# Kernel optimization log

Hardware: AMD Instinct MI355X
Metric: run time of the kernel (lower is better)

## Reference

```python
import jax, jax.numpy as jnp
import numpy as np

CHANNELS = 64
NUM_HEADS = 8
HEAD_DIM = 64
TOTAL_DIM = NUM_HEADS * HEAD_DIM  # 512
FF_DIM = 1024


def setup_inputs() -> dict:
    key = jax.random.key(0)
    ks = jax.random.split(key, 11)
    def lin(kw, kb, out_d, in_d):
        s = 1.0 / np.sqrt(in_d)
        W = jax.random.uniform(kw, (out_d, in_d), jnp.float32, -s, s)
        b = jax.random.uniform(kb, (out_d,), jnp.float32, -s, s)
        return W, b
    x = jax.random.normal(ks[0], (2, CHANNELS, 64, 32), jnp.float32)
    Wq, bq = lin(ks[1], ks[2], TOTAL_DIM, CHANNELS)
    Wk, bk = lin(ks[3], ks[4], TOTAL_DIM, CHANNELS)
    Wv, bv = lin(ks[5], ks[6], TOTAL_DIM, CHANNELS)
    W1, b1 = lin(ks[7], ks[8], FF_DIM, TOTAL_DIM)
    W2, b2 = lin(ks[9], ks[10], CHANNELS, FF_DIM)
    return {"x": x, "Wq": Wq, "bq": bq, "Wk": Wk, "bk": bk,
            "Wv": Wv, "bv": bv, "W1": W1, "b1": b1, "W2": W2, "b2": b2}


def reference(x, Wq, bq, Wk, bk, Wv, bv, W1, b1, W2, b2):
    N, C, H, W = x.shape
    S = H * W
    # [N, S, C]
    x_flat = x.reshape(N, C, S).transpose(0, 2, 1)
    def heads(y):  # [N,S,total] -> [N,h,S,d]
        return y.reshape(N, S, NUM_HEADS, HEAD_DIM).transpose(0, 2, 1, 3)
    Q = heads(x_flat @ Wq.T + bq)
    K = heads(x_flat @ Wk.T + bk)
    V = heads(x_flat @ Wv.T + bv)
    scale = HEAD_DIM ** 0.5
    logits = jnp.einsum('bhqd,bhkd->bhqk', Q, K) / scale
    attn = jax.nn.softmax(logits, axis=-1)
    out = jnp.einsum('bhqk,bhkd->bhqd', attn, V)
    out = out.transpose(0, 2, 1, 3).reshape(N, S, TOTAL_DIM)
    ff = jax.nn.relu(out @ W1.T + b1) @ W2.T + b2
    y = x_flat + ff
    return y.transpose(0, 2, 1).reshape(N, C, H, W)
```

## Files before the change

### kernel.cpp

```cpp
#include <hip/hip_runtime.h>
#include <hip/hip_bf16.h>

constexpr int S  = 2048;
constexpr int C  = 64;
constexpr int NH = 8;
constexpr int HD = 64;
constexpr int TD = 512;
constexpr int FF = 1024;
constexpr int NB = 2;
constexpr int SPLIT  = 4;
constexpr int KTILES = S / SPLIT / 64;

typedef __bf16 bf16x8 __attribute__((ext_vector_type(8)));
typedef float  f32x4  __attribute__((ext_vector_type(4)));

__device__ __forceinline__ f32x4 mfma16(bf16x8 a, bf16x8 b, f32x4 c) {
  return __builtin_amdgcn_mfma_f32_16x16x32_bf16(a, b, c, 0, 0, 0);
}

__device__ __forceinline__ unsigned int pack_bf2(float a, float b) {
  unsigned short ua = __builtin_bit_cast(unsigned short, (__bf16)a);
  unsigned short ub = __builtin_bit_cast(unsigned short, (__bf16)b);
  return (unsigned int)ua | ((unsigned int)ub << 16);
}

__device__ __forceinline__ float bfu2f(unsigned short u) {
  return __builtin_bit_cast(float, (unsigned int)u << 16);
}


__device__ __forceinline__ void cvt_panel(const float* __restrict__ src,
                                          __hip_bfloat16* __restrict__ dst,
                                          int off, int Wd) {
  const int w8 = Wd >> 3;
  const int r  = off / w8;
  const int k8 = off - r * w8;
  const float4 v0 = *(const float4*)(src + (size_t)r * Wd + k8 * 8);
  const float4 v1 = *(const float4*)(src + (size_t)r * Wd + k8 * 8 + 4);
  const int dc = ((r >> 4) * (Wd >> 5) + (k8 >> 2)) * 64 + (k8 & 3) * 16 + (r & 15);
  uint4 pk;
  pk.x = pack_bf2(v0.x, v0.y); pk.y = pack_bf2(v0.z, v0.w);
  pk.z = pack_bf2(v1.x, v1.y); pk.w = pack_bf2(v1.z, v1.w);
  *(uint4*)&dst[dc * 8] = pk;
}

__global__ __launch_bounds__(256) void k_pre(
    const float* __restrict__ Wq, const float* __restrict__ Wk,
    const float* __restrict__ Wv, const float* __restrict__ W1,
    const float* __restrict__ W2, const float* __restrict__ x,
    __hip_bfloat16* __restrict__ Wqf, __hip_bfloat16* __restrict__ Wkf,
    __hip_bfloat16* __restrict__ Wvf, __hip_bfloat16* __restrict__ W1f,
    __hip_bfloat16* __restrict__ W2f, __hip_bfloat16* __restrict__ xbf) {
  const int b = blockIdx.x;
  if (b < 336) {
    const int q = b * 256 + threadIdx.x;
    if      (q < 4096)  cvt_panel(Wq, Wqf, q,         C);
    else if (q < 8192)  cvt_panel(Wk, Wkf, q - 4096,  C);
    else if (q < 12288) cvt_panel(Wv, Wvf, q - 8192,  C);
    else if (q < 77824) cvt_panel(W1, W1f, q - 12288, TD);
    else                cvt_panel(W2, W2f, q - 77824, FF);
  } else {
    const int id = (b - 336) * 256 + threadIdx.x;
    const int k8 = id >> 12;
    const int m  = id & 4095;
    const int n  = m >> 11, s = m & 2047;
    float v[8];
    #pragma unroll
    for (int j = 0; j < 8; ++j)
      v[j] = x[(size_t)(n * C + k8 * 8 + j) * S + s];
    const int p = m >> 4, ks = k8 >> 2, l = (m & 15) + (k8 & 3) * 16;
    uint4 pk;
    pk.x = pack_bf2(v[0], v[1]); pk.y = pack_bf2(v[2], v[3]);
    pk.z = pack_bf2(v[4], v[5]); pk.w = pack_bf2(v[6], v[7]);
    *(uint4*)&xbf[((p * 2 + ks) * 64 + l) * 8] = pk;
  }
}

__global__ __launch_bounds__(256) void k_qkv(
    const __hip_bfloat16* __restrict__ xbf,
    const __hip_bfloat16* __restrict__ Wqf, const float* __restrict__ bq,
    const __hip_bfloat16* __restrict__ Wkf, const float* __restrict__ bk,
    const __hip_bfloat16* __restrict__ Wvf, const float* __restrict__ bv,
    __hip_bfloat16* __restrict__ Qf, __hip_bfloat16* __restrict__ Kf,
    __hip_bfloat16* __restrict__ Vf) {
  const int t = threadIdx.x, w = t >> 6, l = t & 63;
  const int c = l & 15, g = l >> 4;
  const int m0 = blockIdx.y * 64 + w * 16;
  const int xcol = blockIdx.x, which = xcol >> 3, h = xcol & 7;

  const __hip_bfloat16* Wf = (which == 0) ? Wqf : (which == 1) ? Wkf : Wvf;
  const float*        bias = (which == 0) ? bq  : (which == 1) ? bk  : bv;

  f32x4 acc[4];
  #pragma unroll
  for (int i = 0; i < 4; ++i) acc[i] = f32x4{0.f, 0.f, 0.f, 0.f};

  #pragma unroll
  for (int ks = 0; ks < 2; ++ks) {
    const bf16x8 af = *(const bf16x8*)&xbf[(((m0 >> 4) * 2 + ks) * 64 + l) * 8];
    #pragma unroll
    for (int dt = 0; dt < 4; ++dt) {
      const bf16x8 wf =
          *(const bf16x8*)&Wf[(((h * 4 + dt) * 2 + ks) * 64 + l) * 8];
      acc[dt] = mfma16(wf, af, acc[dt]);
    }
  }

  const int m = m0 + c;
  const int nb_ = m >> 11, s = m & 2047;
  const size_t hbq = (size_t)(nb_ * 8 + h) * (S * HD);

  if (which < 2) {
    const float scl = (which == 0) ? 0.1803368801f : 1.0f;
    __hip_bfloat16* Of = ((which == 0) ? Qf : Kf) + hbq;
    const int sp16 = s >> 4;
    #pragma unroll
    for (int dt = 0; dt < 4; ++dt) {
      const int ks = dt >> 1;
      const int lw = c + ((dt & 1) * 2 + (g >> 1)) * 16;
      const int jb = (4 * g) & 7;
      const int d0 = dt * 16 + 4 * g;
      uint2 pk;
      pk.x = pack_bf2((acc[dt][0] + bias[h * 64 + d0 + 0]) * scl,
                      (acc[dt][1] + bias[h * 64 + d0 + 1]) * scl);
      pk.y = pack_bf2((acc[dt][2] + bias[h * 64 + d0 + 2]) * scl,
                      (acc[dt][3] + bias[h * 64 + d0 + 3]) * scl);
      *(uint2*)&Of[((sp16 * 2 + ks) * 64 + lw) * 8 + jb] = pk;
    }
  } else {
    __hip_bfloat16* Vfh = Vf + hbq;
    const int kc = s >> 5, jj = s & 7, lhi = ((s & 31) >> 3) * 16;
    #pragma unroll
    for (int dt = 0; dt < 4; ++dt)
      #pragma unroll
      for (int r = 0; r < 4; ++r) {
        const float v = acc[dt][r] + bias[h * 64 + dt * 16 + 4 * g + r];
        Vfh[((dt * 64 + kc) * 64 + (4 * g + r + lhi)) * 8 + jj] =
            __float2bfloat16(v);
      }
  }
}

__global__ __launch_bounds__(128, 4) void k_attn(
    const __hip_bfloat16* __restrict__ Qf,
    const __hip_bfloat16* __restrict__ Kf,
    const __hip_bfloat16* __restrict__ Vf,
    __hip_bfloat16* __restrict__ Opart, float* __restrict__ Lpart) {
  __shared__ unsigned short P_lds[2][2][2][16][72];

  const int t = threadIdx.x, w = t >> 6, l = t & 63;
  const int c = l & 15, g = l >> 4;
  const int bid = blockIdx.x;
  const int hb  = bid & 15;
  const int sp  = (bid >> 4) & (SPLIT - 1);
  const int q0  = (bid >> 6) * 64 + w * 32;
  const size_t hbase = (size_t)hb * (S * HD);

  bf16x8 qf[2][2];
  const int qp0 = q0 >> 4;
  #pragma unroll
  for (int qq = 0; qq < 2; ++qq)
    #pragma unroll
    for (int ks = 0; ks < 2; ++ks)
      qf[qq][ks] =
          *(const bf16x8*)&Qf[hbase + (((qp0 + qq) * 2 + ks) * 64 + l) * 8];

  f32x4 o[2][4];
  #pragma unroll
  for (int qq = 0; qq < 2; ++qq)
    #pragma unroll
    for (int i = 0; i < 4; ++i) o[qq][i] = f32x4{0.f, 0.f, 0.f, 0.f};
  float lp[2] = {0.f, 0.f};

  const int kb = sp * (S / SPLIT);

  #pragma unroll
  for (int it = 0; it < KTILES; ++it) {
    const int k0  = kb + it * 64;
    const int par = it & 1;
    const int kp0 = k0 >> 4, kc0 = k0 >> 5;

    f32x4 st[2][4];
    #pragma unroll
    for (int qq = 0; qq < 2; ++qq)
      #pragma unroll
      for (int i = 0; i < 4; ++i) st[qq][i] = f32x4{0.f, 0.f, 0.f, 0.f};
    #pragma unroll
    for (int t4 = 0; t4 < 4; ++t4) {
      const bf16x8 ka0 =
          *(const bf16x8*)&Kf[hbase + (((kp0 + t4) * 2 + 0) * 64 + l) * 8];
      const bf16x8 ka1 =
          *(const bf16x8*)&Kf[hbase + (((kp0 + t4) * 2 + 1) * 64 + l) * 8];
      st[0][t4] = mfma16(ka0, qf[0][0], st[0][t4]);
      st[0][t4] = mfma16(ka1, qf[0][1], st[0][t4]);
      st[1][t4] = mfma16(ka0, qf[1][0], st[1][t4]);
      st[1][t4] = mfma16(ka1, qf[1][1], st[1][t4]);
    }

    #pragma unroll
    for (int qq = 0; qq < 2; ++qq)
      #pragma unroll
      for (int t4 = 0; t4 < 4; ++t4) {
        const float e0 = __builtin_amdgcn_exp2f(st[qq][t4][0]);
        const float e1 = __builtin_amdgcn_exp2f(st[qq][t4][1]);
        const float e2 = __builtin_amdgcn_exp2f(st[qq][t4][2]);
        const float e3 = __builtin_amdgcn_exp2f(st[qq][t4][3]);
        lp[qq] += (e0 + e1) + (e2 + e3);
        uint2 pk;
        pk.x = pack_bf2(e0, e1);
        pk.y = pack_bf2(e2, e3);
        *(uint2*)&P_lds[par][w][qq][c][t4 * 16 + g * 4] = pk;
      }

    __builtin_amdgcn_wave_barrier();

    #pragma unroll
    for (int ks = 0; ks < 2; ++ks) {
      const bf16x8 pf0 = *(const bf16x8*)&P_lds[par][w][0][c][ks * 32 + g * 8];
      const bf16x8 pf1 = *(const bf16x8*)&P_lds[par][w][1][c][ks * 32 + g * 8];
      #pragma unroll
      for (int dt = 0; dt < 4; ++dt) {
        const bf16x8 vfr =
            *(const bf16x8*)&Vf[hbase + ((dt * 64 + kc0 + ks) * 64 + l) * 8];
        o[0][dt] = mfma16(pf0, vfr, o[0][dt]);
        o[1][dt] = mfma16(pf1, vfr, o[1][dt]);
      }
    }
  }

  #pragma unroll
  for (int qq = 0; qq < 2; ++qq) {
    lp[qq] += __shfl_xor(lp[qq], 16);
    lp[qq] += __shfl_xor(lp[qq], 32);
  }

  const size_t prow = ((size_t)sp * 16 + hb) * S;
  #pragma unroll
  for (int qq = 0; qq < 2; ++qq) {
    #pragma unroll
    for (int r = 0; r < 4; ++r) {
      __hip_bfloat16* Op = Opart + (prow + q0 + qq * 16 + 4 * g + r) * HD + c;
      Op[0]  = __float2bfloat16(o[qq][0][r]);
      Op[16] = __float2bfloat16(o[qq][1][r]);
      Op[32] = __float2bfloat16(o[qq][2][r]);
      Op[48] = __float2bfloat16(o[qq][3][r]);
    }
    if (l < 16) Lpart[prow + q0 + qq * 16 + l] = lp[qq];
  }
}

__global__ __launch_bounds__(256) void k_comb(
    const __hip_bfloat16* __restrict__ Opart,
    const float* __restrict__ Lpart,
    __hip_bfloat16* __restrict__ ATf) {
  const int gid = blockIdx.x * 256 + threadIdx.x;
  const int r = gid >> 4, dq = (gid & 15) * 4;
  constexpr size_t OSP = (size_t)16 * S * HD;
  constexpr size_t LSP = (size_t)16 * S;

  float l = 0.f;
  float s0 = 0.f, s1 = 0.f, s2 = 0.f, s3 = 0.f;
  #pragma unroll
  for (int sp = 0; sp < SPLIT; ++sp) {
    l += Lpart[sp * LSP + r];
    const ushort4 u = *(const ushort4*)&Opart[sp * OSP + (size_t)r * HD + dq];
    s0 += bfu2f(u.x); s1 += bfu2f(u.y); s2 += bfu2f(u.z); s3 += bfu2f(u.w);
  }
  const float inv = 1.0f / l;

  const int hb = r >> 11, q = r & 2047;
  const int n = hb >> 3, h = hb & 7;
  const int m = n * S + q, k = h * 64 + dq;
  const int mp = m >> 4, ks = k >> 5;
  const int lw = (m & 15) + ((k & 31) >> 3) * 16, j = k & 7;
  uint2 pk;
  pk.x = pack_bf2(s0 * inv, s1 * inv);
  pk.y = pack_bf2(s2 * inv, s3 * inv);
  *(uint2*)&ATf[((mp * 16 + ks) * 64 + lw) * 8 + j] = pk;
}

__global__ __launch_bounds__(256) void k_ff1(
    const __hip_bfloat16* __restrict__ ATf,
    const __hip_bfloat16* __restrict__ W1f,
    const float* __restrict__ b1,
    __hip_bfloat16* __restrict__ F1f) {
  const int t = threadIdx.x, w = t >> 6, l = t & 63;
  const int c = l & 15, g = l >> 4;
  const int mp = blockIdx.y * 4 + w;
  const int bx = blockIdx.x;

  f32x4 acc[8];
  #pragma unroll
  for (int i = 0; i < 8; ++i) acc[i] = f32x4{0.f, 0.f, 0.f, 0.f};

  #pragma unroll
  for (int ks = 0; ks < 16; ++ks) {
    const bf16x8 af = *(const bf16x8*)&ATf[((mp * 16 + ks) * 64 + l) * 8];
    #pragma unroll
    for (int dt = 0; dt < 8; ++dt) {
      const bf16x8 wf =
          *(const bf16x8*)&W1f[(((bx * 8 + dt) * 16 + ks) * 64 + l) * 8];
      acc[dt] = mfma16(wf, af, acc[dt]);
    }
  }

  #pragma unroll
  for (int dt = 0; dt < 8; ++dt) {
    const int ks2 = bx * 4 + (dt >> 1);
    const int lw  = c + ((dt & 1) * 2 + (g >> 1)) * 16;
    const int jb  = (4 * g) & 7;
    const int nn  = bx * 128 + dt * 16 + 4 * g;
    uint2 pk;
    pk.x = pack_bf2(fmaxf(acc[dt][0] + b1[nn + 0], 0.f),
                    fmaxf(acc[dt][1] + b1[nn + 1], 0.f));
    pk.y = pack_bf2(fmaxf(acc[dt][2] + b1[nn + 2], 0.f),
                    fmaxf(acc[dt][3] + b1[nn + 3], 0.f));
    *(uint2*)&F1f[((mp * 32 + ks2) * 64 + lw) * 8 + jb] = pk;
  }
}

__global__ __launch_bounds__(128) void k_ff2(
    const __hip_bfloat16* __restrict__ F1f,
    const __hip_bfloat16* __restrict__ W2f,
    const float* __restrict__ b2,
    const float* __restrict__ x,
    float* __restrict__ out) {
  __shared__ float ot[64][33];
  const int t = threadIdx.x, w = t >> 6, l = t & 63;
  const int c = l & 15, g = l >> 4;
  const int mp = blockIdx.x * 2 + w;

  f32x4 acc[4];
  #pragma unroll
  for (int i = 0; i < 4; ++i) acc[i] = f32x4{0.f, 0.f, 0.f, 0.f};

  #pragma unroll 8
  for (int ks = 0; ks < 32; ++ks) {
    const bf16x8 af = *(const bf16x8*)&F1f[((mp * 32 + ks) * 64 + l) * 8];
    #pragma unroll
    for (int dt = 0; dt < 4; ++dt) {
      const bf16x8 wf = *(const bf16x8*)&W2f[((dt * 32 + ks) * 64 + l) * 8];
      acc[dt] = mfma16(wf, af, acc[dt]);
    }
  }

  #pragma unroll
  for (int dt = 0; dt < 4; ++dt)
    #pragma unroll
    for (int r = 0; r < 4; ++r)
      ot[dt * 16 + 4 * g + r][w * 16 + c] = acc[dt][r];
  __syncthreads();

  const int ch = t >> 1, half = t & 1;
  const int m0 = blockIdx.x * 32;
  const int n = m0 >> 11, s0 = (m0 & 2047) + half * 16;
  const size_t base = ((size_t)n * C + ch) * S + s0;
  const float bb = b2[ch];
  #pragma unroll
  for (int u = 0; u < 4; ++u) {
    const float4 xv = *(const float4*)&x[base + u * 4];
    float4 ov;
    ov.x = ot[ch][half * 16 + u * 4 + 0] + bb + xv.x;
    ov.y = ot[ch][half * 16 + u * 4 + 1] + bb + xv.y;
    ov.z = ot[ch][half * 16 + u * 4 + 2] + bb + xv.z;
    ov.w = ot[ch][half * 16 + u * 4 + 3] + bb + xv.w;
    *(float4*)&out[base + u * 4] = ov;
  }
}

extern "C" void kernel_launch(void* const* d_in, const int* in_sizes, int n_in,
                              void* d_out, int out_size, void* d_ws, size_t ws_size,
                              hipStream_t stream) {
  const float* x  = (const float*)d_in[0];
  const float* Wq = (const float*)d_in[1];
  const float* bq = (const float*)d_in[2];
  const float* Wk = (const float*)d_in[3];
  const float* bk = (const float*)d_in[4];
  const float* Wv = (const float*)d_in[5];
  const float* bv = (const float*)d_in[6];
  const float* W1 = (const float*)d_in[7];
  const float* b1 = (const float*)d_in[8];
  const float* W2 = (const float*)d_in[9];
  const float* b2 = (const float*)d_in[10];
  float* out = (float*)d_out;

  char* wsb = (char*)d_ws;
  const size_t KB = 1024, MB = 1024 * 1024;
  __hip_bfloat16* xbf = (__hip_bfloat16*)(wsb);
  __hip_bfloat16* Wqf = (__hip_bfloat16*)(wsb + 512 * KB);
  __hip_bfloat16* Wkf = (__hip_bfloat16*)(wsb + 576 * KB);
  __hip_bfloat16* Wvf = (__hip_bfloat16*)(wsb + 640 * KB);
  __hip_bfloat16* W1f = (__hip_bfloat16*)(wsb + 768 * KB);
  __hip_bfloat16* W2f = (__hip_bfloat16*)(wsb + 1792 * KB);
  __hip_bfloat16* Qf  = (__hip_bfloat16*)(wsb + 2  * MB);
  __hip_bfloat16* Kf  = (__hip_bfloat16*)(wsb + 6  * MB);
  __hip_bfloat16* Vf  = (__hip_bfloat16*)(wsb + 10 * MB);
  __hip_bfloat16* ATf = (__hip_bfloat16*)(wsb + 14 * MB);
  __hip_bfloat16* F1f = (__hip_bfloat16*)(wsb + 18 * MB);
  __hip_bfloat16* Opart = (__hip_bfloat16*)(wsb + 26 * MB);
  float*          Lpart = (float*)(wsb + 42 * MB);

  k_pre<<<464, 256, 0, stream>>>(Wq, Wk, Wv, W1, W2, x,
                                 Wqf, Wkf, Wvf, W1f, W2f, xbf);
  k_qkv<<<dim3(24, 64), 256, 0, stream>>>(xbf, Wqf, bq, Wkf, bk, Wvf, bv,
                                          Qf, Kf, Vf);
  k_attn<<<16 * SPLIT * 32, 128, 0, stream>>>(Qf, Kf, Vf, Opart, Lpart);
  k_comb<<<2048, 256, 0, stream>>>(Opart, Lpart, ATf);
  k_ff1<<<dim3(8, 64), 256, 0, stream>>>(ATf, W1f, b1, F1f);
  k_ff2<<<128, 128, 0, stream>>>(F1f, W2f, b2, x, out);
}
```

Measured before the change: 151.4 us.

## Fuse split-combine into FF1, compute softmax row sums via MFMA, retile FF kernels

The split-K combine kernel is removed and its work is folded into FF1. FF1 now loads the partial outputs and row sums, normalises them into an LDS tile, then runs the GEMM with 32 rows per block over half the output columns. In attention, the softmax denominator is now accumulated by an MFMA against a ones vector, replacing the VALU adds and shuffles, and s_setprio hints are added around the MFMA phases. FF2 is retiled to 16 rows per block with 4 waves, one per output-channel tile, to get more blocks. The cost is that each FF1 block recomputes the combine for its rows redundantly (two blocks per row pair), and the ones-MFMA sums the bf16-rounded probabilities rather than the fp32 values.

Result: slower. 156.0 us (+3.1%).

```diff
diff --git a/kernel.cpp b/kernel.cpp
--- a/kernel.cpp
+++ b/kernel.cpp
@@ -24,8 +24,8 @@
   return (unsigned int)ua | ((unsigned int)ub << 16);
 }
 
-__device__ __forceinline__ float bfu2f(unsigned short u) {
-  return __builtin_bit_cast(float, (unsigned int)u << 16);
+__device__ __forceinline__ float bfu2f(unsigned int u) {
+  return __builtin_bit_cast(float, (u & 0xffffu) << 16);
 }
 
 
@@ -156,6 +156,10 @@
   const int q0  = (bid >> 6) * 64 + w * 32;
   const size_t hbase = (size_t)hb * (S * HD);
 
+  bf16x8 ones;
+  #pragma unroll
+  for (int j = 0; j < 8; ++j) ones[j] = (__bf16)1.0f;
+
   bf16x8 qf[2][2];
   const int qp0 = q0 >> 4;
   #pragma unroll
@@ -166,11 +170,13 @@
           *(const bf16x8*)&Qf[hbase + (((qp0 + qq) * 2 + ks) * 64 + l) * 8];
 
   f32x4 o[2][4];
-  #pragma unroll
-  for (int qq = 0; qq < 2; ++qq)
+  f32x4 ol[2];
+  #pragma unroll
+  for (int qq = 0; qq < 2; ++qq) {
+    ol[qq] = f32x4{0.f, 0.f, 0.f, 0.f};
     #pragma unroll
     for (int i = 0; i < 4; ++i) o[qq][i] = f32x4{0.f, 0.f, 0.f, 0.f};
-  float lp[2] = {0.f, 0.f};
+  }
 
   const int kb = sp * (S / SPLIT);
 
@@ -185,6 +191,7 @@
     for (int qq = 0; qq < 2; ++qq)
       #pragma unroll
       for (int i = 0; i < 4; ++i) st[qq][i] = f32x4{0.f, 0.f, 0.f, 0.f};
+    __builtin_amdgcn_s_setprio(1);
     #pragma unroll
     for (int t4 = 0; t4 < 4; ++t4) {
       const bf16x8 ka0 =
@@ -196,6 +203,7 @@
       st[1][t4] = mfma16(ka0, qf[1][0], st[1][t4]);
       st[1][t4] = mfma16(ka1, qf[1][1], st[1][t4]);
     }
+    __builtin_amdgcn_s_setprio(0);
 
     #pragma unroll
     for (int qq = 0; qq < 2; ++qq)
@@ -205,7 +213,6 @@
         const float e1 = __builtin_amdgcn_exp2f(st[qq][t4][1]);
         const float e2 = __builtin_amdgcn_exp2f(st[qq][t4][2]);
         const float e3 = __builtin_amdgcn_exp2f(st[qq][t4][3]);
-        lp[qq] += (e0 + e1) + (e2 + e3);
         uint2 pk;
         pk.x = pack_bf2(e0, e1);
         pk.y = pack_bf2(e2, e3);
@@ -214,10 +221,13 @@
 
     __builtin_amdgcn_wave_barrier();
 
+    __builtin_amdgcn_s_setprio(1);
     #pragma unroll
     for (int ks = 0; ks < 2; ++ks) {
       const bf16x8 pf0 = *(const bf16x8*)&P_lds[par][w][0][c][ks * 32 + g * 8];
       const bf16x8 pf1 = *(const bf16x8*)&P_lds[par][w][1][c][ks * 32 + g * 8];
+      ol[0] = mfma16(pf0, ones, ol[0]);
+      ol[1] = mfma16(pf1, ones, ol[1]);
       #pragma unroll
       for (int dt = 0; dt < 4; ++dt) {
         const bf16x8 vfr =
@@ -226,12 +236,7 @@
         o[1][dt] = mfma16(pf1, vfr, o[1][dt]);
       }
     }
-  }
-
-  #pragma unroll
-  for (int qq = 0; qq < 2; ++qq) {
-    lp[qq] += __shfl_xor(lp[qq], 16);
-    lp[qq] += __shfl_xor(lp[qq], 32);
+    __builtin_amdgcn_s_setprio(0);
   }
 
   const size_t prow = ((size_t)sp * 16 + hb) * S;
@@ -245,127 +250,153 @@
       Op[32] = __float2bfloat16(o[qq][2][r]);
       Op[48] = __float2bfloat16(o[qq][3][r]);
     }
-    if (l < 16) Lpart[prow + q0 + qq * 16 + l] = lp[qq];
-  }
-}
-
-__global__ __launch_bounds__(256) void k_comb(
+    if (c == 0) {
+      #pragma unroll
+      for (int r = 0; r < 4; ++r)
+        Lpart[prow + q0 + qq * 16 + 4 * g + r] = ol[qq][r];
+    }
+  }
+}
+
+__global__ __launch_bounds__(256) void k_ff1(
     const __hip_bfloat16* __restrict__ Opart,
     const float* __restrict__ Lpart,
-    __hip_bfloat16* __restrict__ ATf) {
-  const int gid = blockIdx.x * 256 + threadIdx.x;
-  const int r = gid >> 4, dq = (gid & 15) * 4;
-  constexpr size_t OSP = (size_t)16 * S * HD;
-  constexpr size_t LSP = (size_t)16 * S;
-
-  float l = 0.f;
-  float s0 = 0.f, s1 = 0.f, s2 = 0.f, s3 = 0.f;
-  #pragma unroll
-  for (int sp = 0; sp < SPLIT; ++sp) {
-    l += Lpart[sp * LSP + r];
-    const ushort4 u = *(const ushort4*)&Opart[sp * OSP + (size_t)r * HD + dq];
-    s0 += bfu2f(u.x); s1 += bfu2f(u.y); s2 += bfu2f(u.z); s3 += bfu2f(u.w);
-  }
-  const float inv = 1.0f / l;
-
-  const int hb = r >> 11, q = r & 2047;
-  const int n = hb >> 3, h = hb & 7;
-  const int m = n * S + q, k = h * 64 + dq;
-  const int mp = m >> 4, ks = k >> 5;
-  const int lw = (m & 15) + ((k & 31) >> 3) * 16, j = k & 7;
-  uint2 pk;
-  pk.x = pack_bf2(s0 * inv, s1 * inv);
-  pk.y = pack_bf2(s2 * inv, s3 * inv);
-  *(uint2*)&ATf[((mp * 16 + ks) * 64 + lw) * 8 + j] = pk;
-}
-
-__global__ __launch_bounds__(256) void k_ff1(
-    const __hip_bfloat16* __restrict__ ATf,
     const __hip_bfloat16* __restrict__ W1f,
     const float* __restrict__ b1,
     __hip_bfloat16* __restrict__ F1f) {
-  const int t = threadIdx.x, w = t >> 6, l = t & 63;
+  __shared__ __hip_bfloat16 Asm[2][16][64][8];
+  __shared__ float linv_lds[32][8];
+  const int tid = threadIdx.x;
+  const int bid = blockIdx.x;
+  const int mp2 = bid >> 1;
+  const int nh  = bid & 1;
+  constexpr size_t LSP = (size_t)16 * S;
+  constexpr size_t OSP = (size_t)16 * S * HD;
+
+  {
+    const int rr = tid >> 3;
+    const int h  = tid & 7;
+    const int m  = mp2 * 32 + rr;
+    const int n  = m >> 11, q = m & 2047;
+    float lt = 0.f;
+    #pragma unroll
+    for (int sp = 0; sp < SPLIT; ++sp)
+      lt += Lpart[sp * LSP + (size_t)(n * 8 + h) * 2048 + q];
+    linv_lds[rr][h] = 1.0f / lt;
+  }
+  __syncthreads();
+
+  #pragma unroll
+  for (int it = 0; it < 8; ++it) {
+    const int gi = it * 256 + tid;
+    const int pp = gi >> 10;
+    const int ks = (gi >> 6) & 15;
+    const int ll = gi & 63;
+    const int rr = ll & 15, gg = ll >> 4;
+    const int m = mp2 * 32 + pp * 16 + rr;
+    const int n = m >> 11, q = m & 2047;
+    const int h = ks >> 1;
+    const int d0 = (ks & 1) * 32 + gg * 8;
+    const float linv = linv_lds[pp * 16 + rr][h];
+    float s0 = 0.f, s1 = 0.f, s2 = 0.f, s3 = 0.f,
+          s4 = 0.f, s5 = 0.f, s6 = 0.f, s7 = 0.f;
+    #pragma unroll
+    for (int sp = 0; sp < SPLIT; ++sp) {
+      const uint4 u = *(const uint4*)&Opart[sp * OSP +
+          ((size_t)(n * 8 + h) * 2048 + q) * 64 + d0];
+      s0 += bfu2f(u.x); s1 += bfu2f(u.x >> 16);
+      s2 += bfu2f(u.y); s3 += bfu2f(u.y >> 16);
+      s4 += bfu2f(u.z); s5 += bfu2f(u.z >> 16);
+      s6 += bfu2f(u.w); s7 += bfu2f(u.w >> 16);
+    }
+    uint4 pk;
+    pk.x = pack_bf2(s0 * linv, s1 * linv);
+    pk.y = pack_bf2(s2 * linv, s3 * linv);
+    pk.z = pack_bf2(s4 * linv, s5 * linv);
+    pk.w = pack_bf2(s6 * linv, s7 * linv);
+    *(uint4*)&Asm[pp][ks][ll][0] = pk;
+  }
+  __syncthreads();
+
+  const int w = tid >> 6, l = tid & 63;
   const int c = l & 15, g = l >> 4;
-  const int mp = blockIdx.y * 4 + w;
-  const int bx = blockIdx.x;
-
-  f32x4 acc[8];
-  #pragma unroll
-  for (int i = 0; i < 8; ++i) acc[i] = f32x4{0.f, 0.f, 0.f, 0.f};
-
-  #pragma unroll
+  f32x4 acc[2][8];
+  #pragma unroll
+  for (int pp = 0; pp < 2; ++pp)
+    #pragma unroll
+    for (int i = 0; i < 8; ++i) acc[pp][i] = f32x4{0.f, 0.f, 0.f, 0.f};
+
+  #pragma unroll 4
   for (int ks = 0; ks < 16; ++ks) {
-    const bf16x8 af = *(const bf16x8*)&ATf[((mp * 16 + ks) * 64 + l) * 8];
+    const bf16x8 af0 = *(const bf16x8*)&Asm[0][ks][l][0];
+    const bf16x8 af1 = *(const bf16x8*)&Asm[1][ks][l][0];
     #pragma unroll
     for (int dt = 0; dt < 8; ++dt) {
-      const bf16x8 wf =
-          *(const bf16x8*)&W1f[(((bx * 8 + dt) * 16 + ks) * 64 + l) * 8];
-      acc[dt] = mfma16(wf, af, acc[dt]);
-    }
-  }
-
-  #pragma unroll
-  for (int dt = 0; dt < 8; ++dt) {
-    const int ks2 = bx * 4 + (dt >> 1);
-    const int lw  = c + ((dt & 1) * 2 + (g >> 1)) * 16;
-    const int jb  = (4 * g) & 7;
-    const int nn  = bx * 128 + dt * 16 + 4 * g;
-    uint2 pk;
-    pk.x = pack_bf2(fmaxf(acc[dt][0] + b1[nn + 0], 0.f),
-                    fmaxf(acc[dt][1] + b1[nn + 1], 0.f));
-    pk.y = pack_bf2(fmaxf(acc[dt][2] + b1[nn + 2], 0.f),
-                    fmaxf(acc[dt][3] + b1[nn + 3], 0.f));
-    *(uint2*)&F1f[((mp * 32 + ks2) * 64 + lw) * 8 + jb] = pk;
-  }
-}
-
-__global__ __launch_bounds__(128) void k_ff2(
+      const bf16x8 wf = *(const bf16x8*)&W1f[
+          (((size_t)(nh * 32 + w * 8 + dt) * 16 + ks) * 64 + l) * 8];
+      acc[0][dt] = mfma16(wf, af0, acc[0][dt]);
+      acc[1][dt] = mfma16(wf, af1, acc[1][dt]);
+    }
+  }
+
+  #pragma unroll
+  for (int pp = 0; pp < 2; ++pp) {
+    const int mpo = mp2 * 2 + pp;
+    #pragma unroll
+    for (int dt = 0; dt < 8; ++dt) {
+      const int nn0 = nh * 512 + w * 128 + dt * 16 + 4 * g;
+      const int ks2 = nn0 >> 5;
+      const int lw  = c + ((nn0 & 31) >> 3) * 16;
+      const int jb  = nn0 & 7;
+      uint2 pk;
+      pk.x = pack_bf2(fmaxf(acc[pp][dt][0] + b1[nn0 + 0], 0.f),
+                      fmaxf(acc[pp][dt][1] + b1[nn0 + 1], 0.f));
+      pk.y = pack_bf2(fmaxf(acc[pp][dt][2] + b1[nn0 + 2], 0.f),
+                      fmaxf(acc[pp][dt][3] + b1[nn0 + 3], 0.f));
+      *(uint2*)&F1f[(((size_t)mpo * 32 + ks2) * 64 + lw) * 8 + jb] = pk;
+    }
+  }
+}
+
+__global__ __launch_bounds__(256) void k_ff2(
     const __hip_bfloat16* __restrict__ F1f,
     const __hip_bfloat16* __restrict__ W2f,
     const float* __restrict__ b2,
     const float* __restrict__ x,
     float* __restrict__ out) {
-  __shared__ float ot[64][33];
-  const int t = threadIdx.x, w = t >> 6, l = t & 63;
+  __shared__ float ot[64][17];
+  const int tid = threadIdx.x, w = tid >> 6, l = tid & 63;
   const int c = l & 15, g = l >> 4;
-  const int mp = blockIdx.x * 2 + w;
-
-  f32x4 acc[4];
-  #pragma unroll
-  for (int i = 0; i < 4; ++i) acc[i] = f32x4{0.f, 0.f, 0.f, 0.f};
-
+  const int mp = blockIdx.x;
+
+  f32x4 acc0 = f32x4{0.f, 0.f, 0.f, 0.f};
+  f32x4 acc1 = f32x4{0.f, 0.f, 0.f, 0.f};
   #pragma unroll 8
-  for (int ks = 0; ks < 32; ++ks) {
-    const bf16x8 af = *(const bf16x8*)&F1f[((mp * 32 + ks) * 64 + l) * 8];
-    #pragma unroll
-    for (int dt = 0; dt < 4; ++dt) {
-      const bf16x8 wf = *(const bf16x8*)&W2f[((dt * 32 + ks) * 64 + l) * 8];
-      acc[dt] = mfma16(wf, af, acc[dt]);
-    }
-  }
-
-  #pragma unroll
-  for (int dt = 0; dt < 4; ++dt)
-    #pragma unroll
-    for (int r = 0; r < 4; ++r)
-      ot[dt * 16 + 4 * g + r][w * 16 + c] = acc[dt][r];
+  for (int ks = 0; ks < 32; ks += 2) {
+    const bf16x8 af0 = *(const bf16x8*)&F1f[(((size_t)mp * 32 + ks) * 64 + l) * 8];
+    const bf16x8 wf0 = *(const bf16x8*)&W2f[((w * 32 + ks) * 64 + l) * 8];
+    acc0 = mfma16(wf0, af0, acc0);
+    const bf16x8 af1 = *(const bf16x8*)&F1f[(((size_t)mp * 32 + ks + 1) * 64 + l) * 8];
+    const bf16x8 wf1 = *(const bf16x8*)&W2f[((w * 32 + ks + 1) * 64 + l) * 8];
+    acc1 = mfma16(wf1, af1, acc1);
+  }
+  #pragma unroll
+  for (int r = 0; r < 4; ++r)
+    ot[w * 16 + 4 * g + r][c] = acc0[r] + acc1[r];
   __syncthreads();
 
-  const int ch = t >> 1, half = t & 1;
-  const int m0 = blockIdx.x * 32;
-  const int n = m0 >> 11, s0 = (m0 & 2047) + half * 16;
+  const int ch = tid >> 2, si = (tid & 3) * 4;
+  const int m0 = mp * 16;
+  const int n = m0 >> 11, s0 = (m0 & 2047) + si;
   const size_t base = ((size_t)n * C + ch) * S + s0;
   const float bb = b2[ch];
-  #pragma unroll
-  for (int u = 0; u < 4; ++u) {
-    const float4 xv = *(const float4*)&x[base + u * 4];
-    float4 ov;
-    ov.x = ot[ch][half * 16 + u * 4 + 0] + bb + xv.x;
-    ov.y = ot[ch][half * 16 + u * 4 + 1] + bb + xv.y;
-    ov.z = ot[ch][half * 16 + u * 4 + 2] + bb + xv.z;
-    ov.w = ot[ch][half * 16 + u * 4 + 3] + bb + xv.w;
-    *(float4*)&out[base + u * 4] = ov;
-  }
+  const float4 xv = *(const float4*)&x[base];
+  float4 ov;
+  ov.x = ot[ch][si + 0] + bb + xv.x;
+  ov.y = ot[ch][si + 1] + bb + xv.y;
+  ov.z = ot[ch][si + 2] + bb + xv.z;
+  ov.w = ot[ch][si + 3] + bb + xv.w;
+  *(float4*)&out[base] = ov;
 }
 
 extern "C" void kernel_launch(void* const* d_in, const int* in_sizes, int n_in,
@@ -395,7 +426,6 @@
   __hip_bfloat16* Qf  = (__hip_bfloat16*)(wsb + 2  * MB);
   __hip_bfloat16* Kf  = (__hip_bfloat16*)(wsb + 6  * MB);
   __hip_bfloat16* Vf  = (__hip_bfloat16*)(wsb + 10 * MB);
-  __hip_bfloat16* ATf = (__hip_bfloat16*)(wsb + 14 * MB);
   __hip_bfloat16* F1f = (__hip_bfloat16*)(wsb + 18 * MB);
   __hip_bfloat16* Opart = (__hip_bfloat16*)(wsb + 26 * MB);
   float*          Lpart = (float*)(wsb + 42 * MB);
@@ -405,7 +435,6 @@
   k_qkv<<<dim3(24, 64), 256, 0, stream>>>(xbf, Wqf, bq, Wkf, bk, Wvf, bv,
                                           Qf, Kf, Vf);
   k_attn<<<16 * SPLIT * 32, 128, 0, stream>>>(Qf, Kf, Vf, Opart, Lpart);
-  k_comb<<<2048, 256, 0, stream>>>(Opart, Lpart, ATf);
-  k_ff1<<<dim3(8, 64), 256, 0, stream>>>(ATf, W1f, b1, F1f);
-  k_ff2<<<128, 128, 0, stream>>>(F1f, W2f, b2, x, out);
-}
+  k_ff1<<<256, 256, 0, stream>>>(Opart, Lpart, W1f, b1, F1f);
+  k_ff2<<<256, 256, 0, stream>>>(F1f, W2f, b2, x, out);
+}
```

## Compute softmax row sums via MFMA, add setprio, re-split ff2 across more waves

Applied to the files above, without the earlier changes.

In the attention kernel, the per-lane exp accumulation and cross-lane shuffle reduction are replaced by an extra MFMA of P against a ones vector, so row sums come out of the matrix unit. s_setprio raises wave priority around the MFMA sections. k_ff2 now gives each wave one 16-channel output tile with two accumulators, launching 256 blocks of 256 threads instead of 128 of 128 to increase parallelism. k_comb loads Opart as uint2 rather than ushort4. The ones-MFMA adds matrix work but removes VALU adds and shuffles, and the row sums now come from bf16-rounded P rather than fp32 exps, which slightly changes numerics.

Result: faster. 131.8 us (-12.9%).

```diff
diff --git a/kernel.cpp b/kernel.cpp
--- a/kernel.cpp
+++ b/kernel.cpp
@@ -24,8 +24,8 @@
   return (unsigned int)ua | ((unsigned int)ub << 16);
 }
 
-__device__ __forceinline__ float bfu2f(unsigned short u) {
-  return __builtin_bit_cast(float, (unsigned int)u << 16);
+__device__ __forceinline__ float bfu2f(unsigned int u) {
+  return __builtin_bit_cast(float, (u & 0xffffu) << 16);
 }
 
 
@@ -156,6 +156,10 @@
   const int q0  = (bid >> 6) * 64 + w * 32;
   const size_t hbase = (size_t)hb * (S * HD);
 
+  bf16x8 ones;
+  #pragma unroll
+  for (int j = 0; j < 8; ++j) ones[j] = (__bf16)1.0f;
+
   bf16x8 qf[2][2];
   const int qp0 = q0 >> 4;
   #pragma unroll
@@ -166,11 +170,13 @@
           *(const bf16x8*)&Qf[hbase + (((qp0 + qq) * 2 + ks) * 64 + l) * 8];
 
   f32x4 o[2][4];
-  #pragma unroll
-  for (int qq = 0; qq < 2; ++qq)
+  f32x4 ol[2];
+  #pragma unroll
+  for (int qq = 0; qq < 2; ++qq) {
+    ol[qq] = f32x4{0.f, 0.f, 0.f, 0.f};
     #pragma unroll
     for (int i = 0; i < 4; ++i) o[qq][i] = f32x4{0.f, 0.f, 0.f, 0.f};
-  float lp[2] = {0.f, 0.f};
+  }
 
   const int kb = sp * (S / SPLIT);
 
@@ -185,6 +191,7 @@
     for (int qq = 0; qq < 2; ++qq)
       #pragma unroll
       for (int i = 0; i < 4; ++i) st[qq][i] = f32x4{0.f, 0.f, 0.f, 0.f};
+    __builtin_amdgcn_s_setprio(1);
     #pragma unroll
     for (int t4 = 0; t4 < 4; ++t4) {
       const bf16x8 ka0 =
@@ -196,6 +203,7 @@
       st[1][t4] = mfma16(ka0, qf[1][0], st[1][t4]);
       st[1][t4] = mfma16(ka1, qf[1][1], st[1][t4]);
     }
+    __builtin_amdgcn_s_setprio(0);
 
     #pragma unroll
     for (int qq = 0; qq < 2; ++qq)
@@ -205,7 +213,6 @@
         const float e1 = __builtin_amdgcn_exp2f(st[qq][t4][1]);
         const float e2 = __builtin_amdgcn_exp2f(st[qq][t4][2]);
         const float e3 = __builtin_amdgcn_exp2f(st[qq][t4][3]);
-        lp[qq] += (e0 + e1) + (e2 + e3);
         uint2 pk;
         pk.x = pack_bf2(e0, e1);
         pk.y = pack_bf2(e2, e3);
@@ -214,10 +221,13 @@
 
     __builtin_amdgcn_wave_barrier();
 
+    __builtin_amdgcn_s_setprio(1);
     #pragma unroll
     for (int ks = 0; ks < 2; ++ks) {
       const bf16x8 pf0 = *(const bf16x8*)&P_lds[par][w][0][c][ks * 32 + g * 8];
       const bf16x8 pf1 = *(const bf16x8*)&P_lds[par][w][1][c][ks * 32 + g * 8];
+      ol[0] = mfma16(pf0, ones, ol[0]);
+      ol[1] = mfma16(pf1, ones, ol[1]);
       #pragma unroll
       for (int dt = 0; dt < 4; ++dt) {
         const bf16x8 vfr =
@@ -226,12 +236,7 @@
         o[1][dt] = mfma16(pf1, vfr, o[1][dt]);
       }
     }
-  }
-
-  #pragma unroll
-  for (int qq = 0; qq < 2; ++qq) {
-    lp[qq] += __shfl_xor(lp[qq], 16);
-    lp[qq] += __shfl_xor(lp[qq], 32);
+    __builtin_amdgcn_s_setprio(0);
   }
 
   const size_t prow = ((size_t)sp * 16 + hb) * S;
@@ -245,7 +250,11 @@
       Op[32] = __float2bfloat16(o[qq][2][r]);
       Op[48] = __float2bfloat16(o[qq][3][r]);
     }
-    if (l < 16) Lpart[prow + q0 + qq * 16 + l] = lp[qq];
+    if (c == 0) {
+      #pragma unroll
+      for (int r = 0; r < 4; ++r)
+        Lpart[prow + q0 + qq * 16 + 4 * g + r] = ol[qq][r];
+    }
   }
 }
 
@@ -263,8 +272,9 @@
   #pragma unroll
   for (int sp = 0; sp < SPLIT; ++sp) {
     l += Lpart[sp * LSP + r];
-    const ushort4 u = *(const ushort4*)&Opart[sp * OSP + (size_t)r * HD + dq];
-    s0 += bfu2f(u.x); s1 += bfu2f(u.y); s2 += bfu2f(u.z); s3 += bfu2f(u.w);
+    const uint2 u = *(const uint2*)&Opart[sp * OSP + (size_t)r * HD + dq];
+    s0 += bfu2f(u.x); s1 += bfu2f(u.x >> 16);
+    s2 += bfu2f(u.y); s3 += bfu2f(u.y >> 16);
   }
   const float inv = 1.0f / l;
 
@@ -319,53 +329,45 @@
   }
 }
 
-__global__ __launch_bounds__(128) void k_ff2(
+__global__ __launch_bounds__(256) void k_ff2(
     const __hip_bfloat16* __restrict__ F1f,
     const __hip_bfloat16* __restrict__ W2f,
     const float* __restrict__ b2,
     const float* __restrict__ x,
     float* __restrict__ out) {
-  __shared__ float ot[64][33];
-  const int t = threadIdx.x, w = t >> 6, l = t & 63;
+  __shared__ float ot[64][17];
+  const int tid = threadIdx.x, w = tid >> 6, l = tid & 63;
   const int c = l & 15, g = l >> 4;
-  const int mp = blockIdx.x * 2 + w;
-
-  f32x4 acc[4];
-  #pragma unroll
-  for (int i = 0; i < 4; ++i) acc[i] = f32x4{0.f, 0.f, 0.f, 0.f};
-
+  const int mp = blockIdx.x;
+
+  f32x4 acc0 = f32x4{0.f, 0.f, 0.f, 0.f};
+  f32x4 acc1 = f32x4{0.f, 0.f, 0.f, 0.f};
   #pragma unroll 8
-  for (int ks = 0; ks < 32; ++ks) {
-    const bf16x8 af = *(const bf16x8*)&F1f[((mp * 32 + ks) * 64 + l) * 8];
-    #pragma unroll
-    for (int dt = 0; dt < 4; ++dt) {
-      const bf16x8 wf = *(const bf16x8*)&W2f[((dt * 32 + ks) * 64 + l) * 8];
-      acc[dt] = mfma16(wf, af, acc[dt]);
-    }
-  }
-
-  #pragma unroll
-  for (int dt = 0; dt < 4; ++dt)
-    #pragma unroll
-    for (int r = 0; r < 4; ++r)
-      ot[dt * 16 + 4 * g + r][w * 16 + c] = acc[dt][r];
+  for (int ks = 0; ks < 32; ks += 2) {
+    const bf16x8 af0 = *(const bf16x8*)&F1f[(((size_t)mp * 32 + ks) * 64 + l) * 8];
+    const bf16x8 wf0 = *(const bf16x8*)&W2f[((w * 32 + ks) * 64 + l) * 8];
+    acc0 = mfma16(wf0, af0, acc0);
+    const bf16x8 af1 = *(const bf16x8*)&F1f[(((size_t)mp * 32 + ks + 1) * 64 + l) * 8];
+    const bf16x8 wf1 = *(const bf16x8*)&W2f[((w * 32 + ks + 1) * 64 + l) * 8];
+    acc1 = mfma16(wf1, af1, acc1);
+  }
+  #pragma unroll
+  for (int r = 0; r < 4; ++r)
+    ot[w * 16 + 4 * g + r][c] = acc0[r] + acc1[r];
   __syncthreads();
 
-  const int ch = t >> 1, half = t & 1;
-  const int m0 = blockIdx.x * 32;
-  const int n = m0 >> 11, s0 = (m0 & 2047) + half * 16;
+  const int ch = tid >> 2, si = (tid & 3) * 4;
+  const int m0 = mp * 16;
+  const int n = m0 >> 11, s0 = (m0 & 2047) + si;
   const size_t base = ((size_t)n * C + ch) * S + s0;
   const float bb = b2[ch];
-  #pragma unroll
-  for (int u = 0; u < 4; ++u) {
-    const float4 xv = *(const float4*)&x[base + u * 4];
-    float4 ov;
-    ov.x = ot[ch][half * 16 + u * 4 + 0] + bb + xv.x;
-    ov.y = ot[ch][half * 16 + u * 4 + 1] + bb + xv.y;
-    ov.z = ot[ch][half * 16 + u * 4 + 2] + bb + xv.z;
-    ov.w = ot[ch][half * 16 + u * 4 + 3] + bb + xv.w;
-    *(float4*)&out[base + u * 4] = ov;
-  }
+  const float4 xv = *(const float4*)&x[base];
+  float4 ov;
+  ov.x = ot[ch][si + 0] + bb + xv.x;
+  ov.y = ot[ch][si + 1] + bb + xv.y;
+  ov.z = ot[ch][si + 2] + bb + xv.z;
+  ov.w = ot[ch][si + 3] + bb + xv.w;
+  *(float4*)&out[base] = ov;
 }
 
 extern "C" void kernel_launch(void* const* d_in, const int* in_sizes, int n_in,
@@ -407,5 +409,5 @@
   k_attn<<<16 * SPLIT * 32, 128, 0, stream>>>(Qf, Kf, Vf, Opart, Lpart);
   k_comb<<<2048, 256, 0, stream>>>(Opart, Lpart, ATf);
   k_ff1<<<dim3(8, 64), 256, 0, stream>>>(ATf, W1f, b1, F1f);
-  k_ff2<<<128, 128, 0, stream>>>(F1f, W2f, b2, x, out);
-}
+  k_ff2<<<256, 256, 0, stream>>>(F1f, W2f, b2, x, out);
+}
```
